# Kernel optimization log

Hardware: AMD Instinct MI355X
Metric: run time of the kernel (lower is better)

Reference implementation:

```python
import jax, jax.numpy as jnp
import numpy as np

N = 50000      # nodes in current tree level
N_CH = 3       # actual children present in mailbox
D = 4          # max_output_degree
H = 256        # h_size


def setup_inputs() -> dict:
    key = jax.random.key(0)
    ks = jax.random.split(key, 6)
    return {
        "neighbour_h": jax.random.normal(ks[0], (N, N_CH, H), dtype=jnp.float32),
        "neighbour_c": jax.random.normal(ks[1], (N, N_CH, H), dtype=jnp.float32),
        "f_input": jax.random.normal(ks[2], (N, H), dtype=jnp.float32),
        "iou_input": jax.random.normal(ks[3], (N, 3 * H), dtype=jnp.float32),
        # torch nn.Linear convention: weight [out, in]; one per child position
        "U_f": jax.random.normal(ks[4], (D, H, H), dtype=jnp.float32) * 0.05,
        "U_iou": jax.random.normal(ks[5], (D, 3 * H, H), dtype=jnp.float32) * 0.05,
    }


def reference(neighbour_h, neighbour_c, f_input, iou_input, U_f, U_iou):
    n, n_ch, h = neighbour_h.shape
    d = U_f.shape[0]
    pad = d - n_ch
    # check_missing_children: pad with bottom_h / bottom_c == zeros
    nh = jnp.pad(neighbour_h, ((0, 0), (0, pad), (0, 0)))  # [N, D, H]
    nc = jnp.pad(neighbour_c, ((0, 0), (0, pad), (0, 0)))  # [N, D, H]
    # per-position forget gates: U_f_i @ h_i, plus f_input repeated per child
    f_logits = jnp.einsum('ndh,dkh->ndk', nh, U_f) + f_input[:, None, :]
    # iou gate (canonical n-ary tree-LSTM): sum_i U_iou_i @ h_i, plus iou_input
    iou_aggr = jnp.einsum('ndh,dkh->nk', nh, U_iou) + iou_input  # [N, 3H]
    f = jax.nn.sigmoid(f_logits)
    c_aggr = jnp.sum(f * nc, axis=1)  # [N, H]
    # apply_node_func: iou = iou_input + iou_aggr (iou_input counted twice, as in source)
    iou = iou_input + iou_aggr
    i, o, u = jnp.split(iou, 3, axis=1)
    c = jax.nn.sigmoid(i) * jnp.tanh(u) + c_aggr
    h_out = jax.nn.sigmoid(o) * jnp.tanh(c)
    return (h_out, c)
```

## Files before the change

### kernel.cpp

```cpp
#include <hip/hip_runtime.h>
#include <cstdint>
#include <cstddef>

#define NN 50000
#define HD 256
#define NCH 3

typedef __attribute__((ext_vector_type(8))) short shortx8;
typedef __attribute__((ext_vector_type(4))) float floatx4;
typedef __attribute__((ext_vector_type(16))) float floatx16;

__device__ __forceinline__ unsigned short f2bf(float x) {
    union { float f; uint32_t u; } v; v.f = x;
    uint32_t r = v.u + 0x7fffu + ((v.u >> 16) & 1u);
    return (unsigned short)(r >> 16);
}
__device__ __forceinline__ float bf2f(unsigned short u) {
    union { uint32_t u; float f; } v; v.u = ((uint32_t)u) << 16; return v.f;
}
__device__ __forceinline__ uint32_t cvtpk(float a, float b) {
    uint32_t r;
    asm("v_cvt_pk_bf16_f32 %0, %1, %2" : "=v"(r) : "v"(a), "v"(b));
    return r;
}
__device__ __forceinline__ float sigf(float x) {
    return 1.0f / (1.0f + __expf(-x));
}
__device__ __forceinline__ float tanhfast(float x) {
    return 1.0f - 2.0f / (__expf(2.0f * x) + 1.0f);
}
__device__ __forceinline__ floatx16 mfma32(shortx8 a, shortx8 b, floatx16 c) {
    return __builtin_amdgcn_mfma_f32_32x32x16_bf16(a, b, c, 0, 0, 0);
}
__device__ __forceinline__ void glds16(const void* g, void* l) {
    __builtin_amdgcn_global_load_lds(
        (const __attribute__((address_space(1))) void*)g,
        (__attribute__((address_space(3))) void*)l, 16, 0, 0);
}

__global__ void prep_split(const float* __restrict__ U_f,
                           const float* __restrict__ U_iou,
                           unsigned short* __restrict__ wsB) {
    int idx  = blockIdx.x * 256 + threadIdx.x;
    int lane = idx & 63;
    int fg   = idx >> 6;
    const float* src;
    if (fg < 384) {
        int t   = fg >> 4;
        int ksl = fg & 15;
        int d   = t >> 3;
        int c   = t * 32 + (lane & 31) - d * 256;
        int kk  = ksl * 16 + (lane >> 5) * 8;
        src = U_f + ((size_t)d * 256 + c) * 256 + kk;
    } else {
        int fg2 = fg - 384;
        int t2  = fg2 / 48;
        int ksl = fg2 % 48;
        int gc  = t2 * 32 + (lane & 31);
        int g   = gc >> 8;
        int c   = gc & 255;
        int k   = ksl * 16 + (lane >> 5) * 8;
        int d   = k >> 8;
        int kk  = k & 255;
        src = U_iou + ((size_t)d * 768 + g * 256 + c) * 256 + kk;
    }
    shortx8 o;
    #pragma unroll
    for (int e = 0; e < 8; ++e) o[e] = (short)f2bf(src[e]);
    reinterpret_cast<shortx8*>(wsB)[idx] = o;
}

__global__ __launch_bounds__(256) void conv_nh(
    const float* __restrict__ nh, unsigned short* __restrict__ dst,
    int base, int count)
{
    int total = count * 96;
    for (int id = blockIdx.x * 256 + threadIdx.x; id < total;
         id += gridDim.x * 256) {
        int r = id / 96;
        int q = id - r * 96;
        const float4* s4 = reinterpret_cast<const float4*>(
            nh + (size_t)(base + r) * 768 + q * 8);
        float4 a = s4[0], b = s4[1];
        union { uint32_t u[4]; shortx8 v; } o;
        o.u[0] = cvtpk(a.x, a.y); o.u[1] = cvtpk(a.z, a.w);
        o.u[2] = cvtpk(b.x, b.y); o.u[3] = cvtpk(b.z, b.w);
        int S = q >> 3, c = q & 7;
        *reinterpret_cast<shortx8*>(
            dst + (size_t)r * 768 + S * 64 + ((c ^ (r & 7)) * 8)) = o.v;
    }
}

__global__ __launch_bounds__(512, 4) void gemm_logits(
    const unsigned short* __restrict__ nhb,
    const unsigned short* __restrict__ wsB,
    unsigned short* __restrict__ logits,
    int count)
{
    __shared__ unsigned short nhT[2][128 * 64];

    const int tid = threadIdx.x;
    const int bid = blockIdx.x;
    const int cb  = bid % 6;
    const int mb  = bid / 6;
    const int nbl = mb * 128;

    const int lane = tid & 63;
    const int cg   = tid >> 6;
    const int nl   = lane & 31;
    const int hi   = lane >> 5;

    const bool isF    = (cb < 3);
    const int  kbase  = isF ? cb * 256 : 0;
    const int  nsteps = isF ? 4 : 12;
    const int  tF  = cb * 8 + cg;
    const int  t2  = (cb - 3) * 8 + cg;
    const int  fragbase = isF ? (tF * 16) : (384 + t2 * 48);
    const int  colbase  = (isF ? (tF * 32) : (768 + t2 * 32)) + hi * 4;
    const int  clim = count - 1;

    floatx16 acc[4];
    #pragma unroll
    for (int nt = 0; nt < 4; ++nt)
        #pragma unroll
        for (int t = 0; t < 16; ++t) acc[nt][t] = 0.0f;

#define STAGE_NH(S, B)                                                       \
    {                                                                        \
        _Pragma("unroll")                                                    \
        for (int jj = 0; jj < 2; ++jj) {                                     \
            int j    = cg * 2 + jj;                                          \
            int el   = j * 64 + lane;                                        \
            int node = el >> 3;                                               \
            int kk8  = (el & 7) * 8;                                          \
            int row  = nbl + node; if (row > clim) row = clim;               \
            glds16(nhb + (size_t)row * 768 + kbase + (S) * 64 + kk8,         \
                   (void*)(nhT[(B)] + j * 512));                             \
        }                                                                    \
    }

    shortx8 wcur[4], wnxt[4];
    STAGE_NH(0, 0);
    #pragma unroll
    for (int jj = 0; jj < 4; ++jj)
        wcur[jj] = *reinterpret_cast<const shortx8*>(
            wsB + (size_t)(fragbase + jj) * 512 + lane * 8);
    __syncthreads();

    for (int s = 0; s < nsteps; ++s) {
        if (s + 1 < nsteps) {
            STAGE_NH(s + 1, (s + 1) & 1);
            #pragma unroll
            for (int jj = 0; jj < 4; ++jj)
                wnxt[jj] = *reinterpret_cast<const shortx8*>(
                    wsB + (size_t)(fragbase + (s + 1) * 4 + jj) * 512 + lane * 8);
        }

        const unsigned short* buf = nhT[s & 1];
        #pragma unroll
        for (int it = 0; it < 4; ++it) {
            shortx8 a = wcur[it];
            int ch = it * 2 + hi;
            #pragma unroll
            for (int nt = 0; nt < 4; ++nt) {
                int nd = nt * 32 + nl;
                shortx8 b = *reinterpret_cast<const shortx8*>(
                    buf + nd * 64 + ((ch ^ (nl & 7)) * 8));
                acc[nt] = mfma32(a, b, acc[nt]);
            }
        }
        __syncthreads();
        #pragma unroll
        for (int jj = 0; jj < 4; ++jj) wcur[jj] = wnxt[jj];
    }
#undef STAGE_NH

    #pragma unroll
    for (int nt = 0; nt < 4; ++nt) {
        int row = nbl + nt * 32 + nl;
        if (row < count) {
            unsigned short* lr = logits + (size_t)row * 1536;
            #pragma unroll
            for (int q = 0; q < 4; ++q) {
                uint2 wv;
                wv.x = cvtpk(acc[nt][q * 4 + 0], acc[nt][q * 4 + 1]);
                wv.y = cvtpk(acc[nt][q * 4 + 2], acc[nt][q * 4 + 3]);
                *reinterpret_cast<uint2*>(lr + colbase + q * 8) = wv;
            }
        }
    }
}

__global__ __launch_bounds__(256) void ew_kernel(
    const unsigned short* __restrict__ logits,
    const float* __restrict__ ncc,
    const float* __restrict__ f_in,
    const float* __restrict__ iou_in,
    float* __restrict__ out,
    int node_base, int count)
{
    int total = count * 64;
    for (int id = blockIdx.x * 256 + threadIdx.x; id < total;
         id += gridDim.x * 256) {
        int row = id >> 6;
        int col = (id & 63) * 4;
        int gn  = node_base + row;
        const unsigned short* lr = logits + (size_t)row * 1536;

        floatx4 fi = *reinterpret_cast<const floatx4*>(
            f_in + (size_t)gn * HD + col);
        float cagg[4] = {0.f, 0.f, 0.f, 0.f};
        #pragma unroll
        for (int d = 0; d < 3; ++d) {
            ushort4 fb = *reinterpret_cast<const ushort4*>(lr + d * 256 + col);
            floatx4 nc4 = *reinterpret_cast<const floatx4*>(
                ncc + (size_t)gn * 768 + d * 256 + col);
            cagg[0] += sigf(bf2f(fb.x) + fi[0]) * nc4[0];
            cagg[1] += sigf(bf2f(fb.y) + fi[1]) * nc4[1];
            cagg[2] += sigf(bf2f(fb.z) + fi[2]) * nc4[2];
            cagg[3] += sigf(bf2f(fb.w) + fi[3]) * nc4[3];
        }
        ushort4 ib = *reinterpret_cast<const ushort4*>(lr +  768 + col);
        ushort4 ob = *reinterpret_cast<const ushort4*>(lr + 1024 + col);
        ushort4 ub = *reinterpret_cast<const ushort4*>(lr + 1280 + col);
        size_t iob = (size_t)gn * 768 + col;
        floatx4 i4 = *reinterpret_cast<const floatx4*>(iou_in + iob);
        floatx4 o4 = *reinterpret_cast<const floatx4*>(iou_in + iob + 256);
        floatx4 u4 = *reinterpret_cast<const floatx4*>(iou_in + iob + 512);
        float iv[4] = {bf2f(ib.x), bf2f(ib.y), bf2f(ib.z), bf2f(ib.w)};
        float ov[4] = {bf2f(ob.x), bf2f(ob.y), bf2f(ob.z), bf2f(ob.w)};
        float uv[4] = {bf2f(ub.x), bf2f(ub.y), bf2f(ub.z), bf2f(ub.w)};
        floatx4 cc, hh;
        #pragma unroll
        for (int r = 0; r < 4; ++r) {
            float c = sigf(iv[r] + 2.0f * i4[r]) * tanhfast(uv[r] + 2.0f * u4[r])
                      + cagg[r];
            cc[r] = c;
            hh[r] = sigf(ov[r] + 2.0f * o4[r]) * tanhfast(c);
        }
        *reinterpret_cast<floatx4*>(out + (size_t)gn * HD + col) = hh;
        *reinterpret_cast<floatx4*>(out + (size_t)(NN + gn) * HD + col) = cc;
    }
}

__global__ void prep_fused32(const float* __restrict__ U_f,
                             const float* __restrict__ U_iou,
                             unsigned short* __restrict__ wsB) {
    int idx = blockIdx.x * 256 + threadIdx.x;
    int lane = idx & 63;
    int ks   = (idx >> 6) & 15;
    int tile = (idx >> 10) & 31;
    int d    = idx >> 15;
    if (d >= NCH) return;
    int col = tile * 32 + (lane & 31);
    int k0  = ks * 16 + (lane >> 5) * 8;
    const float* src = (col < 256)
        ? (U_f   + (((size_t)d * 256 + col)         * 256 + k0))
        : (U_iou + (((size_t)d * 768 + (col - 256)) * 256 + k0));
    shortx8 o;
    #pragma unroll
    for (int e = 0; e < 8; ++e) o[e] = (short)f2bf(src[e]);
    reinterpret_cast<shortx8*>(wsB)[idx] = o;
}

__global__ __launch_bounds__(512, 4) void fused_main(
    const float* __restrict__ nh, const float* __restrict__ ncc,
    const float* __restrict__ f_in, const float* __restrict__ iou_in,
    const unsigned short* __restrict__ wsB, float* __restrict__ out)
{
    __shared__ unsigned short sA[NCH * 32 * 32 * 8];
    const int tid  = threadIdx.x;
    const int nb   = blockIdx.x * 32;
    const int lane = tid & 63;
    const int cg   = tid >> 6;
    const int nl   = lane & 31;
    const int hi   = lane >> 5;
    const int colb = cg * 32 + hi * 4;
    const shortx8* Bfr = reinterpret_cast<const shortx8*>(wsB);
    #pragma unroll
    for (int i = 0; i < 6; ++i) {
        int c = i * 512 + tid;
        int d = c >> 10, node = (c >> 5) & 31, slot = c & 31;
        int gn = nb + node;
        shortx8 o;
        if (gn < NN) {
            const float4* q = reinterpret_cast<const float4*>(
                nh + ((size_t)gn * (NCH * HD) + d * HD + slot * 8));
            float4 a = q[0], b = q[1];
            union { uint32_t u[4]; shortx8 v; } t;
            t.u[0] = cvtpk(a.x, a.y); t.u[1] = cvtpk(a.z, a.w);
            t.u[2] = cvtpk(b.x, b.y); t.u[3] = cvtpk(b.z, b.w);
            o = t.v;
        } else {
            for (int e = 0; e < 8; ++e) o[e] = 0;
        }
        int idx = (d * 32 + node) * 32 + (slot ^ (node & 7));
        *reinterpret_cast<shortx8*>(&sA[idx * 8]) = o;
    }
    __syncthreads();
    const int  n     = nb + nl;
    const bool valid = (n < NN);
    const int  nc_   = valid ? n : (NN - 1);
    ushort4 finb[4];
    #pragma unroll
    for (int q = 0; q < 4; ++q) {
        floatx4 v = *reinterpret_cast<const floatx4*>(
            f_in + (size_t)nc_ * HD + colb + q * 8);
        finb[q] = ushort4{f2bf(v[0]), f2bf(v[1]), f2bf(v[2]), f2bf(v[3])};
    }
    float cagg[16];
    #pragma unroll
    for (int t = 0; t < 16; ++t) cagg[t] = 0.0f;
    floatx16 accI, accO, accU;
    #pragma unroll
    for (int t = 0; t < 16; ++t) { accI[t] = 0.f; accO[t] = 0.f; accU[t] = 0.f; }
    const int nsw = nl & 7;
    #pragma unroll 1
    for (int d = 0; d < NCH; ++d) {
        floatx16 accF;
        #pragma unroll
        for (int t = 0; t < 16; ++t) accF[t] = 0.0f;
        #pragma unroll 2
        for (int ks = 0; ks < 16; ++ks) {
            shortx8 aF = Bfr[((d * 32 +      cg) * 16 + ks) * 64 + lane];
            shortx8 aI = Bfr[((d * 32 +  8 + cg) * 16 + ks) * 64 + lane];
            shortx8 aO = Bfr[((d * 32 + 16 + cg) * 16 + ks) * 64 + lane];
            shortx8 aU = Bfr[((d * 32 + 24 + cg) * 16 + ks) * 64 + lane];
            int ch = (ks * 2 + hi) ^ nsw;
            shortx8 b = *reinterpret_cast<const shortx8*>(
                &sA[((d * 32 + nl) * 32 + ch) * 8]);
            accF = mfma32(aF, b, accF);
            accI = mfma32(aI, b, accI);
            accO = mfma32(aO, b, accO);
            accU = mfma32(aU, b, accU);
        }
        #pragma unroll
        for (int q = 0; q < 4; ++q) {
            floatx4 ncr = *reinterpret_cast<const floatx4*>(
                ncc + (size_t)nc_ * (NCH * HD) + d * HD + colb + q * 8);
            cagg[q*4+0] += sigf(accF[q*4+0] + bf2f(finb[q].x)) * ncr[0];
            cagg[q*4+1] += sigf(accF[q*4+1] + bf2f(finb[q].y)) * ncr[1];
            cagg[q*4+2] += sigf(accF[q*4+2] + bf2f(finb[q].z)) * ncr[2];
            cagg[q*4+3] += sigf(accF[q*4+3] + bf2f(finb[q].w)) * ncr[3];
        }
    }
    if (valid) {
        #pragma unroll
        for (int q = 0; q < 4; ++q) {
            int col = colb + q * 8;
            size_t base = (size_t)n * 768 + col;
            floatx4 i4 = *reinterpret_cast<const floatx4*>(iou_in + base);
            floatx4 o4 = *reinterpret_cast<const floatx4*>(iou_in + base + 256);
            floatx4 u4 = *reinterpret_cast<const floatx4*>(iou_in + base + 512);
            floatx4 cc, hh;
            #pragma unroll
            for (int r = 0; r < 4; ++r) {
                int t = q * 4 + r;
                float c = sigf(accI[t] + 2.f*i4[r]) * tanhfast(accU[t] + 2.f*u4[r])
                          + cagg[t];
                cc[r] = c;
                hh[r] = sigf(accO[t] + 2.f*o4[r]) * tanhfast(c);
            }
            *reinterpret_cast<floatx4*>(out + (size_t)n * HD + col) = hh;
            *reinterpret_cast<floatx4*>(out + (size_t)(NN + n) * HD + col) = cc;
        }
    }
}

extern "C" void kernel_launch(void* const* d_in, const int* in_sizes, int n_in,
                              void* d_out, int out_size, void* d_ws, size_t ws_size,
                              hipStream_t stream) {
    const float* nh     = (const float*)d_in[0];
    const float* ncc    = (const float*)d_in[1];
    const float* f_in   = (const float*)d_in[2];
    const float* iou_in = (const float*)d_in[3];
    const float* U_f    = (const float*)d_in[4];
    const float* U_iou  = (const float*)d_in[5];
    unsigned short* wsB = (unsigned short*)d_ws;

    const size_t FRAG_BYTES = (size_t)98304 * 16;
    const size_t DATA_OFF   = (size_t)2 << 20;

    long long cmax = 0;
    if (ws_size > DATA_OFF)
        cmax = (long long)((ws_size - DATA_OFF) / 4608);
    cmax = (cmax / 128) * 128;

    if (cmax >= 128) {
        hipLaunchKernelGGL(prep_split, dim3(384), dim3(256), 0, stream,
                           U_f, U_iou, wsB);
        unsigned short* nhswz  = (unsigned short*)((char*)d_ws + DATA_OFF);
        unsigned short* logits = nhswz + (size_t)cmax * 768;
        int base = 0;
        while (base < NN) {
            long long rem = NN - base;
            int count = (int)(rem < cmax ? rem : cmax);

            int cgrid = (count * 96 + 255) / 256;
            if (cgrid > 2048) cgrid = 2048;
            hipLaunchKernelGGL(conv_nh, dim3(cgrid), dim3(256), 0, stream,
                               nh, nhswz, base, count);

            int nmb = (count + 127) / 128;
            hipLaunchKernelGGL(gemm_logits, dim3(nmb * 6), dim3(512), 0,
                               stream, nhswz, wsB, logits, count);

            int ewgrid = (count * 64 + 255) / 256;
            if (ewgrid > 2048) ewgrid = 2048;
            hipLaunchKernelGGL(ew_kernel, dim3(ewgrid), dim3(256), 0, stream,
                               logits, ncc, f_in, iou_in, (float*)d_out,
                               base, count);
            base += count;
        }
    } else if (ws_size >= FRAG_BYTES) {
        hipLaunchKernelGGL(prep_fused32, dim3(384), dim3(256), 0, stream,
                           U_f, U_iou, wsB);
        hipLaunchKernelGGL(fused_main, dim3((NN + 31) / 32), dim3(512), 0,
                           stream, nh, ncc, f_in, iou_in, wsB, (float*)d_out);
    }
}
```

Measured before the change: 302.1 us.

## Shrink gemm block to 64 nodes, 256 threads, two weight tiles per wave

The logits GEMM block changes from 128 nodes with 8 waves to 64 nodes with 4 waves. Each wave now computes two 32-column weight tiles against two 32-node subtiles, so every LDS activation fragment feeds two MFMAs. The weight-fragment register double buffer is replaced by loading the weights at the start of each step, which may expose global-load latency. Halving the LDS tile doubles the grid and reloads weights per block, trading more global weight traffic for more resident blocks and better reuse of the LDS reads.

```diff
diff --git a/kernel.cpp b/kernel.cpp
--- a/kernel.cpp
+++ b/kernel.cpp
@@ -91,19 +91,19 @@
     }
 }
 
-__global__ __launch_bounds__(512, 4) void gemm_logits(
+__global__ __launch_bounds__(256, 4) void gemm_logits(
     const unsigned short* __restrict__ nhb,
     const unsigned short* __restrict__ wsB,
     unsigned short* __restrict__ logits,
     int count)
 {
-    __shared__ unsigned short nhT[2][128 * 64];
+    __shared__ unsigned short nhT[2][64 * 64];
 
     const int tid = threadIdx.x;
     const int bid = blockIdx.x;
     const int cb  = bid % 6;
     const int mb  = bid / 6;
-    const int nbl = mb * 128;
+    const int nbl = mb * 64;
 
     const int lane = tid & 63;
     const int cg   = tid >> 6;
@@ -113,79 +113,82 @@
     const bool isF    = (cb < 3);
     const int  kbase  = isF ? cb * 256 : 0;
     const int  nsteps = isF ? 4 : 12;
-    const int  tF  = cb * 8 + cg;
-    const int  t2  = (cb - 3) * 8 + cg;
-    const int  fragbase = isF ? (tF * 16) : (384 + t2 * 48);
-    const int  colbase  = (isF ? (tF * 32) : (768 + t2 * 32)) + hi * 4;
+    const int  t0 = (isF ? cb * 8 : (cb - 3) * 8) + cg * 2;
+    const int  fragbase0 = isF ? (t0 * 16)       : (384 + t0 * 48);
+    const int  fragbase1 = isF ? ((t0 + 1) * 16) : (384 + (t0 + 1) * 48);
+    const int  colbase0  = (isF ? (t0 * 32)       : (768 + t0 * 32)) + hi * 4;
+    const int  colbase1  = colbase0 + 32;
     const int  clim = count - 1;
 
-    floatx16 acc[4];
-    #pragma unroll
-    for (int nt = 0; nt < 4; ++nt)
-        #pragma unroll
-        for (int t = 0; t < 16; ++t) acc[nt][t] = 0.0f;
+    floatx16 acc[2][2];
+    #pragma unroll
+    for (int w = 0; w < 2; ++w)
+        #pragma unroll
+        for (int nt = 0; nt < 2; ++nt)
+            #pragma unroll
+            for (int t = 0; t < 16; ++t) acc[w][nt][t] = 0.0f;
 
 #define STAGE_NH(S, B)                                                       \
     {                                                                        \
         _Pragma("unroll")                                                    \
         for (int jj = 0; jj < 2; ++jj) {                                     \
-            int j    = cg * 2 + jj;                                          \
+            int j    = cg * 2 + jj;                  \
             int el   = j * 64 + lane;                                        \
-            int node = el >> 3;                                               \
-            int kk8  = (el & 7) * 8;                                          \
+            int node = el >> 3;                                              \
+            int kk8  = (el & 7) * 8;                                         \
             int row  = nbl + node; if (row > clim) row = clim;               \
             glds16(nhb + (size_t)row * 768 + kbase + (S) * 64 + kk8,         \
                    (void*)(nhT[(B)] + j * 512));                             \
         }                                                                    \
     }
 
-    shortx8 wcur[4], wnxt[4];
     STAGE_NH(0, 0);
-    #pragma unroll
-    for (int jj = 0; jj < 4; ++jj)
-        wcur[jj] = *reinterpret_cast<const shortx8*>(
-            wsB + (size_t)(fragbase + jj) * 512 + lane * 8);
     __syncthreads();
 
     for (int s = 0; s < nsteps; ++s) {
-        if (s + 1 < nsteps) {
-            STAGE_NH(s + 1, (s + 1) & 1);
+        shortx8 a0[4], a1[4];
+        #pragma unroll
+        for (int ch = 0; ch < 4; ++ch) {
+            a0[ch] = *reinterpret_cast<const shortx8*>(
+                wsB + (size_t)(fragbase0 + s * 4 + ch) * 512 + lane * 8);
+            a1[ch] = *reinterpret_cast<const shortx8*>(
+                wsB + (size_t)(fragbase1 + s * 4 + ch) * 512 + lane * 8);
+        }
+
+        if (s + 1 < nsteps) STAGE_NH(s + 1, (s + 1) & 1);
+
+        const unsigned short* buf = nhT[s & 1];
+        #pragma unroll
+        for (int ch = 0; ch < 4; ++ch) {
+            int cc = ch * 2 + hi;
             #pragma unroll
-            for (int jj = 0; jj < 4; ++jj)
-                wnxt[jj] = *reinterpret_cast<const shortx8*>(
-                    wsB + (size_t)(fragbase + (s + 1) * 4 + jj) * 512 + lane * 8);
-        }
-
-        const unsigned short* buf = nhT[s & 1];
-        #pragma unroll
-        for (int it = 0; it < 4; ++it) {
-            shortx8 a = wcur[it];
-            int ch = it * 2 + hi;
-            #pragma unroll
-            for (int nt = 0; nt < 4; ++nt) {
+            for (int nt = 0; nt < 2; ++nt) {
                 int nd = nt * 32 + nl;
                 shortx8 b = *reinterpret_cast<const shortx8*>(
-                    buf + nd * 64 + ((ch ^ (nl & 7)) * 8));
-                acc[nt] = mfma32(a, b, acc[nt]);
+                    buf + nd * 64 + ((cc ^ (nl & 7)) * 8));
+                acc[0][nt] = mfma32(a0[ch], b, acc[0][nt]);
+                acc[1][nt] = mfma32(a1[ch], b, acc[1][nt]);
             }
         }
         __syncthreads();
-        #pragma unroll
-        for (int jj = 0; jj < 4; ++jj) wcur[jj] = wnxt[jj];
     }
 #undef STAGE_NH
 
     #pragma unroll
-    for (int nt = 0; nt < 4; ++nt) {
-        int row = nbl + nt * 32 + nl;
-        if (row < count) {
-            unsigned short* lr = logits + (size_t)row * 1536;
-            #pragma unroll
-            for (int q = 0; q < 4; ++q) {
-                uint2 wv;
-                wv.x = cvtpk(acc[nt][q * 4 + 0], acc[nt][q * 4 + 1]);
-                wv.y = cvtpk(acc[nt][q * 4 + 2], acc[nt][q * 4 + 3]);
-                *reinterpret_cast<uint2*>(lr + colbase + q * 8) = wv;
+    for (int w = 0; w < 2; ++w) {
+        int colbase = (w == 0) ? colbase0 : colbase1;
+        #pragma unroll
+        for (int nt = 0; nt < 2; ++nt) {
+            int row = nbl + nt * 32 + nl;
+            if (row < count) {
+                unsigned short* lr = logits + (size_t)row * 1536;
+                #pragma unroll
+                for (int q = 0; q < 4; ++q) {
+                    uint2 wv;
+                    wv.x = cvtpk(acc[w][nt][q * 4 + 0], acc[w][nt][q * 4 + 1]);
+                    wv.y = cvtpk(acc[w][nt][q * 4 + 2], acc[w][nt][q * 4 + 3]);
+                    *reinterpret_cast<uint2*>(lr + colbase + q * 8) = wv;
+                }
             }
         }
     }
@@ -401,8 +404,8 @@
             hipLaunchKernelGGL(conv_nh, dim3(cgrid), dim3(256), 0, stream,
                                nh, nhswz, base, count);
 
-            int nmb = (count + 127) / 128;
-            hipLaunchKernelGGL(gemm_logits, dim3(nmb * 6), dim3(512), 0,
+            int nmb = (count + 63) / 64;
+            hipLaunchKernelGGL(gemm_logits, dim3(nmb * 6), dim3(256), 0,
                                stream, nhswz, wsB, logits, count);
 
             int ewgrid = (count * 64 + 255) / 256;
```

Result: no change. 303.4 us (+0.4%).
